# Performance work log

Measured on AMD Instinct MI355X. Metric: run time of the kernel, lower is better.

Reference implementation:

```python
import jax, jax.numpy as jnp
import numpy as np

KH, KW = 3, 3
KN = KH * KW  # kernel_n = 9


def _grid_offset(H, W):
    # Faithful to TF build(): stack(meshgrid(ij)).reshape(-1, 2) -- note this
    # interleaves i- and j- grids in an unusual layout; we replicate it exactly.
    init = jnp.stack(jnp.meshgrid(jnp.arange(KH), jnp.arange(KW), indexing='ij'))
    init = init.reshape(-1, 2).astype(jnp.float32)  # (KN, 2)
    ph, pw = (KH - 1) // 2, (KW - 1) // 2
    g = jnp.stack(
        jnp.meshgrid(jnp.arange(-ph, H - ph), jnp.arange(-pw, W - pw), indexing='ij'),
        axis=-1,
    ).astype(jnp.float32)  # (H, W, 2)
    return g[:, :, None, :] + init[None, None]  # (H, W, KN, 2)


def _bilinear_sample(x, coords):
    # x: (B, H, W, C); coords: (B, H, W, KN, 2) with (row, col) float coords.
    B = x.shape[0]
    y, xc = coords[..., 0], coords[..., 1]
    y0 = jnp.floor(y).astype(jnp.int32)
    y1 = jnp.ceil(y).astype(jnp.int32)   # ceil (not floor+1), faithful to TF code
    x0 = jnp.floor(xc).astype(jnp.int32)
    x1 = jnp.ceil(xc).astype(jnp.int32)
    bidx = jnp.arange(B)[:, None, None, None]

    def g(yy, xx):
        return x[bidx, yy, xx]  # (B, H, W, KN, C)

    v_lt = g(y0, x0)
    v_rb = g(y1, x1)
    v_lb = g(y0, x1)  # (lt_row, rb_col) per TF coords_lb
    v_rt = g(y1, x0)  # (rb_row, lt_col) per TF coords_rt
    fy = (y - y0.astype(y.dtype))[..., None]
    fx = (xc - x0.astype(xc.dtype))[..., None]
    v_t = v_lt + (v_rt - v_lt) * fy
    v_b = v_lb + (v_rb - v_lb) * fy
    return v_t + (v_b - v_t) * fx  # (B, H, W, KN, C)


def setup_inputs() -> dict:
    key = jax.random.key(0)
    k1, k2, k3 = jax.random.split(key, 3)
    B, H, W, C, F = 8, 64, 64, 128, 128
    x = jax.random.normal(k1, (B, H, W, C), dtype=jnp.float32)
    offset = jax.random.normal(k2, (B, H, W, 2 * KN), dtype=jnp.float32)
    Wk = jax.random.truncated_normal(k3, -2.0, 2.0, (KN, C, F), dtype=jnp.float32) * 0.02
    b = jnp.zeros((F,), dtype=jnp.float32)
    return {"x": x, "offset": offset, "W": Wk, "b": b}


def reference(x, offset, W, b):
    B, H, Wd, C = x.shape
    coords = _grid_offset(H, Wd)[None] + offset.reshape(B, H, Wd, KN, 2)
    coords = jnp.stack(
        [
            jnp.clip(coords[..., 0], 0.0, float(H - 1)),
            jnp.clip(coords[..., 1], 0.0, float(Wd - 1)),
        ],
        axis=-1,
    )
    deform = _bilinear_sample(x, coords)  # (B, H, W, KN, C)
    # conv3d with (1,1,KN,C,F) filter, VALID == contraction over (KN, C)
    out = jnp.einsum('bhwnc,ncf->bhwf', deform, W) + b
    return out
```

## Files before the change

### kernel.cpp

```cpp
#include <hip/hip_runtime.h>
#include <stdint.h>

#define KN 9
#define CC 128
#define FF 128
#define TM 32
#define NT 256
#define LDK 136

typedef __bf16 bf16x8 __attribute__((ext_vector_type(8)));
typedef float f32x4 __attribute__((ext_vector_type(4)));
typedef unsigned short us8 __attribute__((ext_vector_type(8)));

__constant__ float c_init_i[KN] = {0.f,0.f,1.f,2.f,2.f,1.f,0.f,2.f,1.f};
__constant__ float c_init_j[KN] = {0.f,1.f,1.f,2.f,0.f,2.f,1.f,0.f,2.f};

static __device__ inline float bf2f(unsigned short u) {
    union { unsigned u; float f; } v; v.u = ((unsigned)u) << 16; return v.f;
}

__global__ void prep_kernel(const float* __restrict__ Wk, unsigned short* __restrict__ Wt,
                            const float* __restrict__ x, unsigned short* __restrict__ xb) {
    __shared__ unsigned short t[32][33];
    const int tid = threadIdx.x;
    if (blockIdx.x >= 144) {
        int i = ((blockIdx.x - 144) * 256 + tid) * 8;
        float4 a = *(const float4*)(x + i);
        float4 b = *(const float4*)(x + i + 4);
        us8 o;
        o[0] = __builtin_bit_cast(unsigned short, (__bf16)a.x);
        o[1] = __builtin_bit_cast(unsigned short, (__bf16)a.y);
        o[2] = __builtin_bit_cast(unsigned short, (__bf16)a.z);
        o[3] = __builtin_bit_cast(unsigned short, (__bf16)a.w);
        o[4] = __builtin_bit_cast(unsigned short, (__bf16)b.x);
        o[5] = __builtin_bit_cast(unsigned short, (__bf16)b.y);
        o[6] = __builtin_bit_cast(unsigned short, (__bf16)b.z);
        o[7] = __builtin_bit_cast(unsigned short, (__bf16)b.w);
        *(us8*)(xb + i) = o;
        return;
    }
    const int n  = blockIdx.x >> 4;
    const int tf = blockIdx.x & 3;
    const int tc = (blockIdx.x >> 2) & 3;
    const int g  = tid >> 5;
    const int l  = tid & 31;
#pragma unroll
    for (int r = 0; r < 4; ++r) {
        int cl = g * 4 + r;
        t[cl][l] = __builtin_bit_cast(unsigned short,
                    (__bf16)Wk[(n << 14) + ((tc * 32 + cl) << 7) + (tf * 32 + l)]);
    }
    __syncthreads();
#pragma unroll
    for (int r = 0; r < 4; ++r) {
        int o   = r * 256 + tid;
        int b   = o >> 9;
        int q   = (o >> 7) & 3;
        int col = (o >> 3) & 15;
        int e   = o & 7;
        Wt[(((n * 4 + tc) * 4 + tf) << 10) + o] = t[q * 8 + e][b * 16 + col];
    }
}

#define ISSUE(n_, p_, S) do {                                          \
    int lt_o = cB[p_][n_][0], rb_o = cB[p_][n_][1];                    \
    int rt_o = (rb_o & 0x7E000) | (lt_o & 0x1F80);                     \
    int lb_o = (lt_o & 0x7E000) | (rb_o & 0x1F80);                     \
    lt##S = *(const us8*)(bb16 + lt_o + icg);                          \
    rt##S = *(const us8*)(bb16 + rt_o + icg);                          \
    lb##S = *(const us8*)(bb16 + lb_o + icg);                          \
    rb##S = *(const us8*)(bb16 + rb_o + icg);                          \
    __builtin_amdgcn_sched_barrier(0);                                 \
  } while (0)

#define CONSUME(n_, p_, S, d_) do {                                    \
    float fy_ = cF[p_][n_][0], fx_ = cF[p_][n_][1];                    \
    us8 pk_;                                                           \
    _Pragma("unroll")                                                  \
    for (int j = 0; j < 8; ++j) {                                      \
      float v0_ = bf2f(lt##S[j]), v1_ = bf2f(rt##S[j]);                \
      float v2_ = bf2f(lb##S[j]), v3_ = bf2f(rb##S[j]);                \
      float vt_ = v0_ + (v1_ - v0_) * fy_;                             \
      float vb_ = v2_ + (v3_ - v2_) * fy_;                             \
      float r_  = vt_ + (vb_ - vt_) * fx_;                             \
      pk_[j] = __builtin_bit_cast(unsigned short, (__bf16)r_);         \
    }                                                                  \
    *(us8*)&As[d_][p_][icg] = pk_;                                     \
  } while (0)

#define LOADB(n_) do {                                                 \
    bfr0 = *(const us8*)(wbase + ((n_) << 14));                        \
    bfr1 = *(const us8*)(wbase + ((n_) << 14) + 512);                  \
    bfr2 = *(const us8*)(wbase + ((n_) << 14) + 4096);                 \
    bfr3 = *(const us8*)(wbase + ((n_) << 14) + 4096 + 512);           \
    bfr4 = *(const us8*)(wbase + ((n_) << 14) + 8192);                 \
    bfr5 = *(const us8*)(wbase + ((n_) << 14) + 8192 + 512);           \
    bfr6 = *(const us8*)(wbase + ((n_) << 14) + 12288);                \
    bfr7 = *(const us8*)(wbase + ((n_) << 14) + 12288 + 512);          \
    __builtin_amdgcn_sched_barrier(0);                                 \
  } while (0)

#define MSTEP(d_, ks_, B0, B1) do {                                    \
    bf16x8 a0_ = __builtin_bit_cast(bf16x8, *(const us8*)(&As[d_][col][(ks_) * 32 + quad * 8]));      \
    bf16x8 a1_ = __builtin_bit_cast(bf16x8, *(const us8*)(&As[d_][16 + col][(ks_) * 32 + quad * 8])); \
    acc00 = __builtin_amdgcn_mfma_f32_16x16x32_bf16(a0_, __builtin_bit_cast(bf16x8, B0), acc00, 0, 0, 0); \
    acc01 = __builtin_amdgcn_mfma_f32_16x16x32_bf16(a0_, __builtin_bit_cast(bf16x8, B1), acc01, 0, 0, 0); \
    acc10 = __builtin_amdgcn_mfma_f32_16x16x32_bf16(a1_, __builtin_bit_cast(bf16x8, B0), acc10, 0, 0, 0); \
    acc11 = __builtin_amdgcn_mfma_f32_16x16x32_bf16(a1_, __builtin_bit_cast(bf16x8, B1), acc11, 0, 0, 0); \
  } while (0)

#define MTAP(d_) do {                                                  \
    MSTEP(d_, 0, bfr0, bfr1); MSTEP(d_, 1, bfr2, bfr3);                \
    MSTEP(d_, 2, bfr4, bfr5); MSTEP(d_, 3, bfr6, bfr7);                \
  } while (0)

#define BAR() do {                                                     \
    asm volatile("s_waitcnt lgkmcnt(0)" ::: "memory");                 \
    __builtin_amdgcn_s_barrier();                                      \
  } while (0)

__launch_bounds__(NT, 4)
__global__ void deform_kernel(const unsigned short* __restrict__ xb,
                              const float* __restrict__ off,
                              const unsigned short* __restrict__ Wt,
                              const float* __restrict__ bias,
                              float* __restrict__ out) {
    __shared__ unsigned short As[2][TM][LDK];
    __shared__ int   cB[TM][KN][2];
    __shared__ float cF[TM][KN][2];

    const int tid = threadIdx.x;
    const int bb   = blockIdx.x & 7;
    const int rr   = blockIdx.x >> 3;
    const int pix0 = (bb << 12) + (rr << 5);

    for (int t = tid; t < TM * KN; t += NT) {
        int p = t & (TM - 1);
        int n = t >> 5;
        int pg = (rr << 5) + p;
        float2 o = *(const float2*)(off + (size_t)(pix0 + p) * (2 * KN) + 2 * n);
        float y = (float)((pg >> 6) - 1) + c_init_i[n] + o.x;
        float x = (float)((pg & 63) - 1) + c_init_j[n] + o.y;
        y = fminf(fmaxf(y, 0.f), 63.f);
        x = fminf(fmaxf(x, 0.f), 63.f);
        float y0f = floorf(y), x0f = floorf(x);
        int y0 = (int)y0f, x0 = (int)x0f;
        int y1 = (int)ceilf(y), x1 = (int)ceilf(x);
        cB[p][n][0] = (y0 << 13) | (x0 << 7);
        cB[p][n][1] = (y1 << 13) | (x1 << 7);
        cF[p][n][0] = y - y0f;
        cF[p][n][1] = x - x0f;
    }

    const int wave = tid >> 6;
    const int lane = tid & 63;
    const int quad = lane >> 4;
    const int col  = lane & 15;

    f32x4 acc00 = {0.f,0.f,0.f,0.f}, acc01 = {0.f,0.f,0.f,0.f};
    f32x4 acc10 = {0.f,0.f,0.f,0.f}, acc11 = {0.f,0.f,0.f,0.f};

    const unsigned short* bb16  = xb + ((size_t)bb << 19);
    const unsigned short* wbase = Wt + (wave << 10) + (lane << 3);

    const int ip0 = tid >> 4;
    const int ip1 = ip0 + 16;
    const int icg = (tid & 15) * 8;

    us8 ltA, rtA, lbA, rbA;
    us8 ltB, rtB, lbB, rbB;
    us8 bfr0, bfr1, bfr2, bfr3, bfr4, bfr5, bfr6, bfr7;

    __syncthreads();

    ISSUE(0, ip0, A);
    int d = 0;

    for (int n = 0; n < KN; ++n, d ^= 1) {
        ISSUE(n, ip1, B);
        LOADB(n);
        CONSUME(n, ip0, A, d);
        CONSUME(n, ip1, B, d);

        BAR();

        if (n + 1 < KN) ISSUE(n + 1, ip0, A);

        MTAP(d);
    }

    const int fbase = (wave << 5);
#pragma unroll
    for (int b = 0; b < 2; ++b) {
        int f = fbase + b * 16 + col;
        float bv = bias[f];
        const f32x4 ac0 = b ? acc01 : acc00;
        const f32x4 ac1 = b ? acc11 : acc10;
#pragma unroll
        for (int r = 0; r < 4; ++r) {
            int pr0 = pix0 + (quad << 2) + r;
            out[(size_t)pr0 * FF + f] = ac0[r] + bv;
            int pr1 = pr0 + 16;
            out[(size_t)pr1 * FF + f] = ac1[r] + bv;
        }
    }
}

extern "C" void kernel_launch(void* const* d_in, const int* in_sizes, int n_in,
                              void* d_out, int out_size, void* d_ws, size_t ws_size,
                              hipStream_t stream) {
    const float* x    = (const float*)d_in[0];
    const float* off  = (const float*)d_in[1];
    const float* Wk   = (const float*)d_in[2];
    const float* bias = (const float*)d_in[3];
    float* out = (float*)d_out;
    unsigned short* Wt = (unsigned short*)d_ws;
    unsigned short* xb = (unsigned short*)d_ws + 147456;

    prep_kernel<<<144 + 2048, 256, 0, stream>>>(Wk, Wt, x, xb);
    deform_kernel<<<(8 * 64 * 64) / TM, NT, 0, stream>>>(xb, off, Wt, bias, out);
}
```

Measured before the change: 98.70 us.

## Fuse prep and deform kernels with a global atomic grid barrier

Merges the bf16 conversion of x and the weight transpose into the main deformable-conv kernel. Each of the 1024 blocks converts its own slice of x, the first 144 also convert weights, and then all blocks wait on a global atomic counter before gathering. This removes one kernel launch and the gap between launches, but adds a memset and a spin barrier. The barrier relies on all 1024 blocks being co-resident, which the launch bounds of 4 blocks per CU should allow. It also has a timeout guard that could let blocks proceed before the data is ready.

```diff
diff --git a/kernel.cpp b/kernel.cpp
--- a/kernel.cpp
+++ b/kernel.cpp
@@ -7,6 +7,7 @@
 #define TM 32
 #define NT 256
 #define LDK 136
+#define NBLK 1024
 
 typedef __bf16 bf16x8 __attribute__((ext_vector_type(8)));
 typedef float f32x4 __attribute__((ext_vector_type(4)));
@@ -17,49 +18,6 @@
 
 static __device__ inline float bf2f(unsigned short u) {
     union { unsigned u; float f; } v; v.u = ((unsigned)u) << 16; return v.f;
-}
-
-__global__ void prep_kernel(const float* __restrict__ Wk, unsigned short* __restrict__ Wt,
-                            const float* __restrict__ x, unsigned short* __restrict__ xb) {
-    __shared__ unsigned short t[32][33];
-    const int tid = threadIdx.x;
-    if (blockIdx.x >= 144) {
-        int i = ((blockIdx.x - 144) * 256 + tid) * 8;
-        float4 a = *(const float4*)(x + i);
-        float4 b = *(const float4*)(x + i + 4);
-        us8 o;
-        o[0] = __builtin_bit_cast(unsigned short, (__bf16)a.x);
-        o[1] = __builtin_bit_cast(unsigned short, (__bf16)a.y);
-        o[2] = __builtin_bit_cast(unsigned short, (__bf16)a.z);
-        o[3] = __builtin_bit_cast(unsigned short, (__bf16)a.w);
-        o[4] = __builtin_bit_cast(unsigned short, (__bf16)b.x);
-        o[5] = __builtin_bit_cast(unsigned short, (__bf16)b.y);
-        o[6] = __builtin_bit_cast(unsigned short, (__bf16)b.z);
-        o[7] = __builtin_bit_cast(unsigned short, (__bf16)b.w);
-        *(us8*)(xb + i) = o;
-        return;
-    }
-    const int n  = blockIdx.x >> 4;
-    const int tf = blockIdx.x & 3;
-    const int tc = (blockIdx.x >> 2) & 3;
-    const int g  = tid >> 5;
-    const int l  = tid & 31;
-#pragma unroll
-    for (int r = 0; r < 4; ++r) {
-        int cl = g * 4 + r;
-        t[cl][l] = __builtin_bit_cast(unsigned short,
-                    (__bf16)Wk[(n << 14) + ((tc * 32 + cl) << 7) + (tf * 32 + l)]);
-    }
-    __syncthreads();
-#pragma unroll
-    for (int r = 0; r < 4; ++r) {
-        int o   = r * 256 + tid;
-        int b   = o >> 9;
-        int q   = (o >> 7) & 3;
-        int col = (o >> 3) & 15;
-        int e   = o & 7;
-        Wt[(((n * 4 + tc) * 4 + tf) << 10) + o] = t[q * 8 + e][b * 16 + col];
-    }
 }
 
 #define ISSUE(n_, p_, S) do {                                          \
@@ -120,37 +78,106 @@
   } while (0)
 
 __launch_bounds__(NT, 4)
-__global__ void deform_kernel(const unsigned short* __restrict__ xb,
-                              const float* __restrict__ off,
-                              const unsigned short* __restrict__ Wt,
-                              const float* __restrict__ bias,
-                              float* __restrict__ out) {
+__global__ void fused_kernel(const float* __restrict__ x,
+                             const float* __restrict__ off,
+                             const float* __restrict__ Wk,
+                             const float* __restrict__ bias,
+                             float* __restrict__ out,
+                             unsigned short* __restrict__ Wt,
+                             unsigned short* __restrict__ xb,
+                             unsigned int* __restrict__ flag) {
     __shared__ unsigned short As[2][TM][LDK];
     __shared__ int   cB[TM][KN][2];
     __shared__ float cF[TM][KN][2];
+    __shared__ unsigned short t[32][33];
 
     const int tid = threadIdx.x;
-    const int bb   = blockIdx.x & 7;
-    const int rr   = blockIdx.x >> 3;
+    const int blk = blockIdx.x;
+    const int bb   = blk & 7;
+    const int rr   = blk >> 3;
     const int pix0 = (bb << 12) + (rr << 5);
 
-    for (int t = tid; t < TM * KN; t += NT) {
-        int p = t & (TM - 1);
-        int n = t >> 5;
+    {
+        const int base = (bb << 19) + (rr << 12) + tid * 16;
+        float4 a0 = *(const float4*)(x + base);
+        float4 a1 = *(const float4*)(x + base + 4);
+        float4 a2 = *(const float4*)(x + base + 8);
+        float4 a3 = *(const float4*)(x + base + 12);
+        us8 o0, o1;
+        o0[0] = __builtin_bit_cast(unsigned short, (__bf16)a0.x);
+        o0[1] = __builtin_bit_cast(unsigned short, (__bf16)a0.y);
+        o0[2] = __builtin_bit_cast(unsigned short, (__bf16)a0.z);
+        o0[3] = __builtin_bit_cast(unsigned short, (__bf16)a0.w);
+        o0[4] = __builtin_bit_cast(unsigned short, (__bf16)a1.x);
+        o0[5] = __builtin_bit_cast(unsigned short, (__bf16)a1.y);
+        o0[6] = __builtin_bit_cast(unsigned short, (__bf16)a1.z);
+        o0[7] = __builtin_bit_cast(unsigned short, (__bf16)a1.w);
+        o1[0] = __builtin_bit_cast(unsigned short, (__bf16)a2.x);
+        o1[1] = __builtin_bit_cast(unsigned short, (__bf16)a2.y);
+        o1[2] = __builtin_bit_cast(unsigned short, (__bf16)a2.z);
+        o1[3] = __builtin_bit_cast(unsigned short, (__bf16)a2.w);
+        o1[4] = __builtin_bit_cast(unsigned short, (__bf16)a3.x);
+        o1[5] = __builtin_bit_cast(unsigned short, (__bf16)a3.y);
+        o1[6] = __builtin_bit_cast(unsigned short, (__bf16)a3.z);
+        o1[7] = __builtin_bit_cast(unsigned short, (__bf16)a3.w);
+        *(us8*)(xb + base)     = o0;
+        *(us8*)(xb + base + 8) = o1;
+    }
+
+    if (blk < 144) {
+        const int n  = blk >> 4;
+        const int tf = blk & 3;
+        const int tc = (blk >> 2) & 3;
+        const int g  = tid >> 5;
+        const int l  = tid & 31;
+#pragma unroll
+        for (int r = 0; r < 4; ++r) {
+            int cl = g * 4 + r;
+            t[cl][l] = __builtin_bit_cast(unsigned short,
+                        (__bf16)Wk[(n << 14) + ((tc * 32 + cl) << 7) + (tf * 32 + l)]);
+        }
+        __syncthreads();
+#pragma unroll
+        for (int r = 0; r < 4; ++r) {
+            int o   = r * 256 + tid;
+            int b   = o >> 9;
+            int q   = (o >> 7) & 3;
+            int col = (o >> 3) & 15;
+            int e   = o & 7;
+            Wt[(((n * 4 + tc) * 4 + tf) << 10) + o] = t[q * 8 + e][b * 16 + col];
+        }
+    }
+
+    for (int tt = tid; tt < TM * KN; tt += NT) {
+        int p = tt & (TM - 1);
+        int n = tt >> 5;
         int pg = (rr << 5) + p;
         float2 o = *(const float2*)(off + (size_t)(pix0 + p) * (2 * KN) + 2 * n);
-        float y = (float)((pg >> 6) - 1) + c_init_i[n] + o.x;
-        float x = (float)((pg & 63) - 1) + c_init_j[n] + o.y;
-        y = fminf(fmaxf(y, 0.f), 63.f);
-        x = fminf(fmaxf(x, 0.f), 63.f);
-        float y0f = floorf(y), x0f = floorf(x);
+        float y  = (float)((pg >> 6) - 1) + c_init_i[n] + o.x;
+        float xx = (float)((pg & 63) - 1) + c_init_j[n] + o.y;
+        y  = fminf(fmaxf(y, 0.f), 63.f);
+        xx = fminf(fmaxf(xx, 0.f), 63.f);
+        float y0f = floorf(y), x0f = floorf(xx);
         int y0 = (int)y0f, x0 = (int)x0f;
-        int y1 = (int)ceilf(y), x1 = (int)ceilf(x);
+        int y1 = (int)ceilf(y), x1 = (int)ceilf(xx);
         cB[p][n][0] = (y0 << 13) | (x0 << 7);
         cB[p][n][1] = (y1 << 13) | (x1 << 7);
         cF[p][n][0] = y - y0f;
-        cF[p][n][1] = x - x0f;
-    }
+        cF[p][n][1] = xx - x0f;
+    }
+    __syncthreads();
+
+    if (tid == 0) {
+        __threadfence();
+        __hip_atomic_fetch_add(flag, 1u, __ATOMIC_RELEASE, __HIP_MEMORY_SCOPE_AGENT);
+        int guard = 0;
+        while (__hip_atomic_load(flag, __ATOMIC_ACQUIRE, __HIP_MEMORY_SCOPE_AGENT) < NBLK) {
+            __builtin_amdgcn_s_sleep(2);
+            if (++guard > 1000000) break;
+        }
+    }
+    __syncthreads();
+    __threadfence();
 
     const int wave = tid >> 6;
     const int lane = tid & 63;
@@ -170,8 +197,6 @@
     us8 ltA, rtA, lbA, rbA;
     us8 ltB, rtB, lbB, rbB;
     us8 bfr0, bfr1, bfr2, bfr3, bfr4, bfr5, bfr6, bfr7;
-
-    __syncthreads();
 
     ISSUE(0, ip0, A);
     int d = 0;
@@ -216,7 +241,8 @@
     float* out = (float*)d_out;
     unsigned short* Wt = (unsigned short*)d_ws;
     unsigned short* xb = (unsigned short*)d_ws + 147456;
-
-    prep_kernel<<<144 + 2048, 256, 0, stream>>>(Wk, Wt, x, xb);
-    deform_kernel<<<(8 * 64 * 64) / TM, NT, 0, stream>>>(xb, off, Wt, bias, out);
+    unsigned int* flag = (unsigned int*)((char*)d_ws + (16u << 20));
+
+    hipMemsetAsync(flag, 0, 4, stream);
+    fused_kernel<<<NBLK, NT, 0, stream>>>(x, off, Wk, bias, out, Wt, xb, flag);
 }
```

After: 280.8 us. 184% more time.
